# Performance work log

Measured on AMD Instinct MI355X. Metric: run time of the kernel, lower is better.

Reference implementation:

```python
import jax, jax.numpy as jnp
import numpy as np

B, T, V, S = 16, 100, 50000, 4


def setup_inputs() -> dict:
    key = jax.random.key(0)
    k1, k2, k3, k4 = jax.random.split(key, 4)
    output = jax.random.normal(k1, (B, T, V), dtype=jnp.float32)
    labels = jax.random.randint(k2, (B, T), 0, V, dtype=jnp.int32)
    x_lens = jax.random.randint(k3, (B,), 1, T + 1, dtype=jnp.int32)  # >=1 to avoid 0-length users
    uids = jnp.arange(B, dtype=jnp.int32)
    neg_ids = jax.random.randint(k4, (B, T, S), 0, V, dtype=jnp.int32)  # pre-sampled negatives
    return {"output": output, "labels": labels, "x_lens": x_lens, "uids": uids, "neg_ids": neg_ids}


def reference(output, labels, x_lens, uids, neg_ids):
    # output: [B, T, V]; labels: [B, T]; x_lens: [B]; neg_ids: [B, T, S]
    pos = jnp.take_along_axis(output, labels[:, :, None], axis=2)       # [B, T, 1]
    neg = jnp.take_along_axis(output, neg_ids, axis=2)                  # [B, T, S]
    ls = jax.nn.log_sigmoid(pos - neg)                                  # [B, T, S]
    mask = (jnp.arange(output.shape[1])[None, :] < x_lens[:, None])     # [B, T] valid positions
    per_t = ls.sum(axis=-1) * mask.astype(ls.dtype)                     # [B, T]
    per_user = -per_t.sum(axis=1) / x_lens.astype(ls.dtype)             # -mean over valid steps
    return (per_user.sum() / output.shape[0]).reshape(1)
```

## Files before the change

kernel.cpp:

```cpp
#include <hip/hip_runtime.h>
#include <math.h>

#define BB 16
#define TT 100
#define VV 50000
#define SS 4
#define NTHREADS 1024

__global__ __launch_bounds__(NTHREADS)
void bpr_loss_kernel(const float* __restrict__ output,
                     const int*   __restrict__ labels,
                     const int*   __restrict__ x_lens,
                     const int*   __restrict__ neg_ids,
                     float*       __restrict__ out) {
    const int tid = threadIdx.x;

    float acc = 0.0f;

    for (int i = tid; i < BB * TT; i += NTHREADS) {
        const int b = i / TT;
        const int t = i - b * TT;
        const int xl = x_lens[b];
        if (t < xl) {
            const float* row = output + (size_t)i * VV;
            const float  pos = row[labels[i]];
            const int*   nid = neg_ids + (size_t)i * SS;
            float s_sum = 0.0f;
            #pragma unroll
            for (int s = 0; s < SS; ++s) {
                const float neg = row[nid[s]];
                const float x   = pos - neg;
                const float ls  = fminf(x, 0.0f) - log1pf(__expf(-fabsf(x)));
                s_sum += ls;
            }
            acc += s_sum / (float)xl;
        }
    }

    #pragma unroll
    for (int off = 32; off > 0; off >>= 1)
        acc += __shfl_down(acc, off, 64);

    __shared__ float wave_sums[NTHREADS / 64];
    const int wave = tid >> 6;
    if ((tid & 63) == 0) wave_sums[wave] = acc;
    __syncthreads();

    if (tid < NTHREADS / 64) {
        float v = wave_sums[tid];
        #pragma unroll
        for (int off = (NTHREADS / 64) / 2; off > 0; off >>= 1)
            v += __shfl_down(v, off, NTHREADS / 64);
        if (tid == 0)
            out[0] = -v / (float)BB;
    }
}

extern "C" void kernel_launch(void* const* d_in, const int* in_sizes, int n_in,
                              void* d_out, int out_size, void* d_ws, size_t ws_size,
                              hipStream_t stream) {
    const float* output  = (const float*)d_in[0];
    const int*   labels  = (const int*)  d_in[1];
    const int*   x_lens  = (const int*)  d_in[2];
    const int*   neg_ids = (const int*)  d_in[4];
    float*       out     = (float*)d_out;

    bpr_loss_kernel<<<1, NTHREADS, 0, stream>>>(output, labels, x_lens, neg_ids, out);
}
```

Baseline: 11.28 us.

## Split loss into multi-block partial kernel plus final reduction kernel

Replaces the single 1024-thread block with 25 single-wave blocks, each handling 64 (b,t) pairs and writing a partial sum to workspace. A second one-wave kernel then reduces the partials. The idea is to spread the random gathers over many CUs to get more memory-level parallelism, and to load the negative ids as one int4 each. The cost is a second kernel launch and a round trip through global memory for the partials.

```diff
diff --git a/kernel.cpp b/kernel.cpp
--- a/kernel.cpp
+++ b/kernel.cpp
@@ -5,35 +5,42 @@
 #define TT 100
 #define VV 50000
 #define SS 4
-#define NTHREADS 1024
+#define NPAIRS (BB * TT)
+#define NBLK ((NPAIRS + 63) / 64)
 
-__global__ __launch_bounds__(NTHREADS)
-void bpr_loss_kernel(const float* __restrict__ output,
-                     const int*   __restrict__ labels,
-                     const int*   __restrict__ x_lens,
-                     const int*   __restrict__ neg_ids,
-                     float*       __restrict__ out) {
-    const int tid = threadIdx.x;
+__global__ __launch_bounds__(64)
+void bpr_partial_kernel(const float* __restrict__ output,
+                        const int*   __restrict__ labels,
+                        const int*   __restrict__ x_lens,
+                        const int*   __restrict__ neg_ids,
+                        float*       __restrict__ partials) {
+    const int lane = threadIdx.x;
+    const int i    = blockIdx.x * 64 + lane;
 
     float acc = 0.0f;
+    if (i < NPAIRS) {
+        const int  lab = labels[i];
+        const int4 nid = *((const int4*)neg_ids + i);
+        const int  b   = i / TT;
+        const int  t   = i - b * TT;
+        const int  xl  = x_lens[b];
 
-    for (int i = tid; i < BB * TT; i += NTHREADS) {
-        const int b = i / TT;
-        const int t = i - b * TT;
-        const int xl = x_lens[b];
         if (t < xl) {
             const float* row = output + (size_t)i * VV;
-            const float  pos = row[labels[i]];
-            const int*   nid = neg_ids + (size_t)i * SS;
-            float s_sum = 0.0f;
+            const float pos = row[lab];
+            const float n0  = row[nid.x];
+            const float n1  = row[nid.y];
+            const float n2  = row[nid.z];
+            const float n3  = row[nid.w];
+
+            float s = 0.0f;
+            const float xs[4] = {pos - n0, pos - n1, pos - n2, pos - n3};
             #pragma unroll
-            for (int s = 0; s < SS; ++s) {
-                const float neg = row[nid[s]];
-                const float x   = pos - neg;
-                const float ls  = fminf(x, 0.0f) - log1pf(__expf(-fabsf(x)));
-                s_sum += ls;
+            for (int s_i = 0; s_i < SS; ++s_i) {
+                const float x = xs[s_i];
+                s += fminf(x, 0.0f) - log1pf(__expf(-fabsf(x)));
             }
-            acc += s_sum / (float)xl;
+            acc = s / (float)xl;
         }
     }
 
@@ -41,19 +48,20 @@
     for (int off = 32; off > 0; off >>= 1)
         acc += __shfl_down(acc, off, 64);
 
-    __shared__ float wave_sums[NTHREADS / 64];
-    const int wave = tid >> 6;
-    if ((tid & 63) == 0) wave_sums[wave] = acc;
-    __syncthreads();
+    if (lane == 0)
+        partials[blockIdx.x] = acc;
+}
 
-    if (tid < NTHREADS / 64) {
-        float v = wave_sums[tid];
-        #pragma unroll
-        for (int off = (NTHREADS / 64) / 2; off > 0; off >>= 1)
-            v += __shfl_down(v, off, NTHREADS / 64);
-        if (tid == 0)
-            out[0] = -v / (float)BB;
-    }
+__global__ __launch_bounds__(64)
+void bpr_final_kernel(const float* __restrict__ partials,
+                      float*       __restrict__ out) {
+    const int lane = threadIdx.x;
+    float v = (lane < NBLK) ? partials[lane] : 0.0f;
+    #pragma unroll
+    for (int off = 32; off > 0; off >>= 1)
+        v += __shfl_down(v, off, 64);
+    if (lane == 0)
+        out[0] = -v / (float)BB;
 }
 
 extern "C" void kernel_launch(void* const* d_in, const int* in_sizes, int n_in,
@@ -64,6 +72,8 @@
     const int*   x_lens  = (const int*)  d_in[2];
     const int*   neg_ids = (const int*)  d_in[4];
     float*       out     = (float*)d_out;
+    float*       partials = (float*)d_ws;
 
-    bpr_loss_kernel<<<1, NTHREADS, 0, stream>>>(output, labels, x_lens, neg_ids, out);
+    bpr_partial_kernel<<<NBLK, 64, 0, stream>>>(output, labels, x_lens, neg_ids, partials);
+    bpr_final_kernel<<<1, 64, 0, stream>>>(partials, out);
 }
```

New measurement: 10.92 us. 3.3% less time.
